# Kernel optimization log

Hardware: AMD Instinct MI355X
Metric: run time of the kernel (lower is better)

The kernel has to match this reference:

```python
import jax, jax.numpy as jnp
import numpy as np

DN = ('NHWC', 'HWIO', 'NHWC')

def _conv1x1(x, k):
    # 1x1 conv, stride 1, SAME padding (channels_last)
    return jax.lax.conv_general_dilated(x, k, window_strides=(1, 1), padding='SAME', dimension_numbers=DN)

def setup_inputs() -> dict:
    key = jax.random.key(0)
    k1, k2, k3, k4, k5 = jax.random.split(key, 5)
    B, H, W, C = 4, 64, 64, 256
    c8 = C // 8
    x = jax.random.normal(k1, (B, H, W, C), dtype=jnp.float32)
    # Glorot-like scaling for stability
    kernel_f = jax.random.normal(k2, (1, 1, C, c8), dtype=jnp.float32) * (1.0 / np.sqrt(C))
    kernel_g = jax.random.normal(k3, (1, 1, C, c8), dtype=jnp.float32) * (1.0 / np.sqrt(C))
    kernel_h = jax.random.normal(k4, (1, 1, C, C), dtype=jnp.float32) * (1.0 / np.sqrt(C))
    gamma = jax.random.normal(k5, (), dtype=jnp.float32) * 0.1
    return {'x': x, 'kernel_f': kernel_f, 'kernel_g': kernel_g, 'kernel_h': kernel_h, 'gamma': gamma}

def reference(x, kernel_f, kernel_g, kernel_h, gamma):
    B, H, W, C = x.shape
    N = H * W
    f = _conv1x1(x, kernel_f).reshape(B, N, -1)   # [B, N, C/8] queries
    g = _conv1x1(x, kernel_g).reshape(B, N, -1)   # [B, N, C/8] keys
    h = _conv1x1(x, kernel_h).reshape(B, N, -1)   # [B, N, C]   values
    e = jnp.einsum('bnc,bmc->bnm', f, g)          # [B, N, N] scores
    attn = jax.nn.softmax(e, axis=-1)
    o = jnp.einsum('bnm,bmc->bnc', attn, h).reshape(B, H, W, C)
    return x + gamma * o
```

## Files before the change

kernel.cpp:

```cpp
#include <hip/hip_runtime.h>

typedef __attribute__((ext_vector_type(8))) short bf16x8;
typedef __attribute__((ext_vector_type(4))) float f32x4;
typedef __attribute__((ext_vector_type(16))) float f32x16;

__device__ __forceinline__ unsigned short f2bf(float f) {
    union { float f; unsigned u; } v; v.f = f;
    return (unsigned short)((v.u + 0x7FFFu + ((v.u >> 16) & 1u)) >> 16);
}

__device__ __forceinline__ float fexp2(float v) {
#if __has_builtin(__builtin_amdgcn_exp2f)
    return __builtin_amdgcn_exp2f(v);
#else
    float r; asm("v_exp_f32 %0, %1" : "=v"(r) : "v"(v)); return r;
#endif
}
__device__ __forceinline__ unsigned cvt_pk_bf16(float lo, float hi) {
    unsigned r;
    asm("v_cvt_pk_bf16_f32 %0, %1, %2" : "=v"(r) : "v"(lo), "v"(hi));
    return r;
}

__device__ __forceinline__ void async16(unsigned short* lds, const unsigned short* gsrc) {
    __builtin_amdgcn_global_load_lds(
        (const __attribute__((address_space(1))) void*)gsrc,
        (__attribute__((address_space(3))) void*)lds, 16, 0, 0);
}

__global__ __launch_bounds__(256) void k_wt(const float* __restrict__ kf,
                                            const float* __restrict__ kg,
                                            const float* __restrict__ kh,
                                            unsigned short* __restrict__ wt) {
    int n = blockIdx.x, t = threadIdx.x;
    const float* src; int stride, col;
    if (n < 32)      { src = kf; stride = 32;  col = n; }
    else if (n < 64) { src = kg; stride = 32;  col = n - 32; }
    else             { src = kh; stride = 256; col = n - 64; }
    float v = src[t * stride + col];
    if (n < 32) v *= 1.44269504088896341f;
    wt[n * 256 + (((t >> 3) ^ (n & 7)) << 3) + (t & 7)] = f2bf(v);
}

__global__ __launch_bounds__(512) void k_proj(const float* __restrict__ x,
                                              const unsigned short* __restrict__ wt,
                                              unsigned short* __restrict__ f,
                                              unsigned short* __restrict__ g,
                                              unsigned short* __restrict__ hT) {
    __shared__ unsigned short xs[16384];
    __shared__ unsigned short ws[2][16384];
    int t = threadIdx.x, rb = blockIdx.x;
    int w = t >> 6, lane = t & 63, q = lane >> 4, n15 = lane & 15;
    int b = rb >> 6, nbase = (rb & 63) * 64;

#pragma unroll
    for (int i = 0; i < 8; ++i) {
        int lin = i * 512 + t, row = lin >> 6, c4 = lin & 63;
        float4 v = *(const float4*)&x[(rb * 64 + row) * 256 + c4 * 4];
        ushort4 o; o.x = f2bf(v.x); o.y = f2bf(v.y); o.z = f2bf(v.z); o.w = f2bf(v.w);
        *(ushort4*)&xs[row * 256 + (((c4 >> 1) ^ (row & 7)) << 3) + ((c4 & 1) << 2)] = o;
    }
#pragma unroll
    for (int j = 0; j < 4; ++j)
        async16(&ws[0][(j * 512 + w * 64) * 8], wt + (j * 512 + t) * 8);

    for (int ct = 0; ct < 5; ++ct) {
        int cur = ct & 1, nxt = cur ^ 1;
        __syncthreads();
        if (ct < 4) {
            const unsigned short* wsrc = wt + (ct + 1) * 16384;
#pragma unroll
            for (int j = 0; j < 4; ++j)
                async16(&ws[nxt][(j * 512 + w * 64) * 8], wsrc + (j * 512 + t) * 8);
        }
        const unsigned short* wcur = ws[cur];
        f32x4 acc[2];
        acc[0] = (f32x4){0.f, 0.f, 0.f, 0.f};
        acc[1] = (f32x4){0.f, 0.f, 0.f, 0.f};

        if (ct == 0) {
            int rg = w & 3, cg = w >> 2;
#pragma unroll
            for (int kk = 0; kk < 8; ++kk) {
                bf16x8 a = *(const bf16x8*)&xs[(rg * 16 + n15) * 256
                                + ((((kk << 2) + q) ^ (n15 & 7)) << 3)];
#pragma unroll
                for (int nt = 0; nt < 2; ++nt) {
                    bf16x8 bw = *(const bf16x8*)&wcur[(cg * 32 + nt * 16 + n15) * 256
                                    + ((((kk << 2) + q) ^ (n15 & 7)) << 3)];
                    acc[nt] = __builtin_amdgcn_mfma_f32_16x16x32_bf16(a, bw, acc[nt], 0, 0, 0);
                }
            }
#pragma unroll
            for (int nt = 0; nt < 2; ++nt)
#pragma unroll
                for (int r = 0; r < 4; ++r) {
                    int grow = rb * 64 + rg * 16 + q * 4 + r;
                    int col = cg * 32 + nt * 16 + n15;
                    unsigned short v = f2bf(acc[nt][r]);
                    if (col < 32) f[grow * 32 + col] = v;
                    else          g[grow * 32 + (col - 32)] = v;
                }
        } else {
            int cg = w & 3, rg = w >> 2;
#pragma unroll
            for (int kk = 0; kk < 8; ++kk) {
                bf16x8 a = *(const bf16x8*)&wcur[(cg * 16 + n15) * 256
                                + ((((kk << 2) + q) ^ (n15 & 7)) << 3)];
#pragma unroll
                for (int nt = 0; nt < 2; ++nt) {
                    bf16x8 bx = *(const bf16x8*)&xs[(rg * 32 + nt * 16 + n15) * 256
                                    + ((((kk << 2) + q) ^ (n15 & 7)) << 3)];
                    acc[nt] = __builtin_amdgcn_mfma_f32_16x16x32_bf16(a, bx, acc[nt], 0, 0, 0);
                }
            }
#pragma unroll
            for (int nt = 0; nt < 2; ++nt)
#pragma unroll
                for (int r = 0; r < 4; ++r) {
                    int ch = (ct - 1) * 64 + cg * 16 + q * 4 + r;
                    int nloc = nbase + rg * 32 + nt * 16 + n15;
                    hT[b * 1048576 + ch * 4096 + nloc] = f2bf(acc[nt][r]);
                }
        }
    }
}

__global__ __launch_bounds__(512, 4) void k_attn(const float* __restrict__ x,
                                                 const unsigned short* __restrict__ f,
                                                 const unsigned short* __restrict__ g,
                                                 const unsigned short* __restrict__ hT,
                                                 const float* __restrict__ gamma_p,
                                                 float* __restrict__ out) {
    __shared__ unsigned short hs[3][8192];
    __shared__ unsigned short pls[2][4096];
    __shared__ float lpart[4][64];
    __shared__ __align__(16) float lrec[64];
    int t = threadIdx.x, bx = blockIdx.x;
    int b = (bx >> 1) & 3;
    int ch2 = (bx >> 3) & 1;
    int qt = ((bx & 1) << 5) | (bx >> 4);
    int qbase = qt * 64;
    int chbase = ch2 * 128;
    int w = t >> 6, l = t & 63;
    int hi = l >> 5, l31 = l & 31;
    int q = l >> 4, n15 = l & 15;
    int cb = w & 3;
    const bool is_s = (w < 4);

    bf16x8 aFB[4];
    const unsigned short* gW = g + (b * 4096 + w * 16 + n15) * 32 + q * 8;
    if (is_s) {
#pragma unroll
        for (int nt = 0; nt < 4; ++nt)
            aFB[nt] = *(const bf16x8*)&f[(b * 4096 + qbase + nt * 16 + n15) * 32 + q * 8];
    }
    bf16x8 aG, aGn;
    f32x4 lac = (f32x4){0.f, 0.f, 0.f, 0.f};
    const f32x4 zero4 = (f32x4){0.f, 0.f, 0.f, 0.f};

    const unsigned short* hsrc = hT + b * 1048576 + (chbase + (t >> 3)) * 4096
                               + (((t & 7) ^ ((t >> 3) & 7)) << 3);

    auto s_tile = [&](int buf) {
        f32x4 sa[4];
#pragma unroll
        for (int nt = 0; nt < 4; ++nt)
            sa[nt] = __builtin_amdgcn_mfma_f32_16x16x32_bf16(aG, aFB[nt], zero4, 0, 0, 0);
        int kq = w * 4 + q;
#pragma unroll
        for (int nt = 0; nt < 4; ++nt) {
#pragma unroll
            for (int r = 0; r < 4; ++r) {
                sa[nt][r] = fexp2(sa[nt][r]);
                lac[nt] += sa[nt][r];
            }
            unsigned p0 = cvt_pk_bf16(sa[nt][0], sa[nt][1]);
            unsigned p1 = cvt_pk_bf16(sa[nt][2], sa[nt][3]);
            int row = nt * 16 + n15;
            unsigned* dst = (unsigned*)&pls[buf][row * 64]
                          + (((kq >> 1) ^ (n15 & 7)) << 2) + ((kq & 1) << 1);
            dst[0] = p0; dst[1] = p1;
        }
    };

    f32x16 o0, o1;
#pragma unroll
    for (int i = 0; i < 16; ++i) { o0[i] = 0.f; o1[i] = 0.f; }

    async16(&hs[0][w * 512], hsrc);
    async16(&hs[0][4096 + w * 512], hsrc + 64 * 4096);
    async16(&hs[1][w * 512], hsrc + 64);
    async16(&hs[1][4096 + w * 512], hsrc + 64 * 4096 + 64);
    if (is_s) {
        aG  = *(const bf16x8*)&gW[0];
        aGn = *(const bf16x8*)&gW[2048];
        s_tile(0);
        aG = aGn;
        __builtin_amdgcn_sched_barrier(0);
        asm volatile("s_waitcnt vmcnt(3) lgkmcnt(0)" ::: "memory");
    } else {
        __builtin_amdgcn_sched_barrier(0);
        asm volatile("s_waitcnt vmcnt(2)" ::: "memory");
    }
    __builtin_amdgcn_s_barrier();
    __builtin_amdgcn_sched_barrier(0);

    for (int kt = 0; kt < 64; ++kt) {
        int cur = kt & 1, nxt = cur ^ 1;
        int h_cur = kt % 3, h_nxt2 = (kt + 2) % 3;
        const bool more = (kt + 2 < 64);

        if (more) {
            const unsigned short* hp = hsrc + (kt + 2) * 64;
            async16(&hs[h_nxt2][w * 512], hp);
            async16(&hs[h_nxt2][4096 + w * 512], hp + 64 * 4096);
        }

        if (is_s) {
            if (kt + 1 < 64) {
                int ktn = (kt + 2 < 64) ? kt + 2 : 63;
                aGn = *(const bf16x8*)&gW[ktn * 2048];
                s_tile(nxt);
                aG = aGn;
            }
            __builtin_amdgcn_sched_barrier(0);
            if (more) asm volatile("s_waitcnt vmcnt(3) lgkmcnt(0)" ::: "memory");
            else      asm volatile("s_waitcnt vmcnt(1) lgkmcnt(0)" ::: "memory");
        } else {
            const unsigned short* hcur = &hs[h_cur][0];
            const unsigned short* pcur = &pls[cur][0];
            __builtin_amdgcn_s_setprio(1);
#pragma unroll
            for (int ks = 0; ks < 4; ++ks) {
                int seg = (((2 * ks + hi) ^ (l31 & 7)) << 3);
                bf16x8 bH  = *(const bf16x8*)&hcur[(cb * 32 + l31) * 64 + seg];
                bf16x8 aP0 = *(const bf16x8*)&pcur[l31 * 64 + seg];
                bf16x8 aP1 = *(const bf16x8*)&pcur[(32 + l31) * 64 + seg];
                o0 = __builtin_amdgcn_mfma_f32_32x32x16_bf16(aP0, bH, o0, 0, 0, 0);
                o1 = __builtin_amdgcn_mfma_f32_32x32x16_bf16(aP1, bH, o1, 0, 0, 0);
            }
            __builtin_amdgcn_s_setprio(0);
            __builtin_amdgcn_sched_barrier(0);
            if (more) asm volatile("s_waitcnt vmcnt(2)" ::: "memory");
            else      asm volatile("s_waitcnt vmcnt(0)" ::: "memory");
        }

        __builtin_amdgcn_s_barrier();
        __builtin_amdgcn_sched_barrier(0);
    }

    if (is_s) {
#pragma unroll
        for (int nt = 0; nt < 4; ++nt) {
            float ps = lac[nt];
            ps += __shfl_xor(ps, 16);
            ps += __shfl_xor(ps, 32);
            if (q == 0) lpart[w][nt * 16 + n15] = ps;
        }
    }
    __syncthreads();
    if (t < 64) lrec[t] = 1.0f / (lpart[0][t] + lpart[1][t] + lpart[2][t] + lpart[3][t]);
    __syncthreads();
    if (!is_s) {
        float gam = *gamma_p;
        int ch = chbase + cb * 32 + l31;
#pragma unroll
        for (int qq = 0; qq < 4; ++qq) {
            int r0 = 8 * qq + 4 * hi;
            f32x4 ri0 = *(const f32x4*)&lrec[r0];
            f32x4 ri1 = *(const f32x4*)&lrec[32 + r0];
#pragma unroll
            for (int j = 0; j < 4; ++j) {
                int idx0 = (b * 4096 + qbase + r0 + j) * 256 + ch;
                int idx1 = idx0 + 32 * 256;
                out[idx0] = x[idx0] + gam * (o0[4 * qq + j] * ri0[j]);
                out[idx1] = x[idx1] + gam * (o1[4 * qq + j] * ri1[j]);
            }
        }
    }
}

extern "C" void kernel_launch(void* const* d_in, const int* in_sizes, int n_in,
                              void* d_out, int out_size, void* d_ws, size_t ws_size,
                              hipStream_t stream) {
    const float* x  = (const float*)d_in[0];
    const float* kf = (const float*)d_in[1];
    const float* kg = (const float*)d_in[2];
    const float* kh = (const float*)d_in[3];
    const float* gm = (const float*)d_in[4];
    float* out = (float*)d_out;

    char* ws = (char*)d_ws;
    unsigned short* wt = (unsigned short*)(ws);
    unsigned short* fb = (unsigned short*)(ws + 163840);
    unsigned short* gb = (unsigned short*)(ws + 1212416);
    unsigned short* hT = (unsigned short*)(ws + 2260992);

    hipLaunchKernelGGL(k_wt,   dim3(320), dim3(256), 0, stream, kf, kg, kh, wt);
    hipLaunchKernelGGL(k_proj, dim3(256), dim3(512), 0, stream, x, wt, fb, gb, hT);
    hipLaunchKernelGGL(k_attn, dim3(512), dim3(512), 0, stream, x, fb, gb, hT, gm, out);
}
```

Baseline: 144.8 us.

## Halve projection row tile to double grid and single-buffer weight tiles

The projection kernel now processes 32 rows per block instead of 64 and launches 512 blocks instead of 256. Each wave computes one MFMA tile per stage instead of two. The weight tile buffer in shared memory is single-buffered, with the next tile loaded after the current compute and an extra barrier. This aims to fill more compute units and cut shared-memory use, at the cost of losing load/compute overlap and refetching the weights for each smaller row tile.

```diff
diff --git a/kernel.cpp b/kernel.cpp
--- a/kernel.cpp
+++ b/kernel.cpp
@@ -47,82 +47,71 @@
                                               unsigned short* __restrict__ f,
                                               unsigned short* __restrict__ g,
                                               unsigned short* __restrict__ hT) {
-    __shared__ unsigned short xs[16384];
-    __shared__ unsigned short ws[2][16384];
+    __shared__ unsigned short xs[8192];
+    __shared__ unsigned short ws[16384];
     int t = threadIdx.x, rb = blockIdx.x;
     int w = t >> 6, lane = t & 63, q = lane >> 4, n15 = lane & 15;
-    int b = rb >> 6, nbase = (rb & 63) * 64;
-
-#pragma unroll
-    for (int i = 0; i < 8; ++i) {
+    int b = rb >> 7, nbase = (rb & 127) * 32;
+    int rg0 = w & 1, cg0 = w >> 1;
+    int cgh = w & 3, rgh = w >> 2;
+
+#pragma unroll
+    for (int i = 0; i < 4; ++i) {
         int lin = i * 512 + t, row = lin >> 6, c4 = lin & 63;
-        float4 v = *(const float4*)&x[(rb * 64 + row) * 256 + c4 * 4];
+        float4 v = *(const float4*)&x[(rb * 32 + row) * 256 + c4 * 4];
         ushort4 o; o.x = f2bf(v.x); o.y = f2bf(v.y); o.z = f2bf(v.z); o.w = f2bf(v.w);
         *(ushort4*)&xs[row * 256 + (((c4 >> 1) ^ (row & 7)) << 3) + ((c4 & 1) << 2)] = o;
     }
 #pragma unroll
     for (int j = 0; j < 4; ++j)
-        async16(&ws[0][(j * 512 + w * 64) * 8], wt + (j * 512 + t) * 8);
+        async16(&ws[(j * 512 + w * 64) * 8], wt + (j * 512 + t) * 8);
+    __syncthreads();
 
     for (int ct = 0; ct < 5; ++ct) {
-        int cur = ct & 1, nxt = cur ^ 1;
+        f32x4 acc = (f32x4){0.f, 0.f, 0.f, 0.f};
+        if (ct == 0) {
+#pragma unroll
+            for (int kk = 0; kk < 8; ++kk) {
+                bf16x8 a = *(const bf16x8*)&xs[(rg0 * 16 + n15) * 256
+                                + ((((kk << 2) + q) ^ (n15 & 7)) << 3)];
+                bf16x8 bw = *(const bf16x8*)&ws[(cg0 * 16 + n15) * 256
+                                + ((((kk << 2) + q) ^ (n15 & 7)) << 3)];
+                acc = __builtin_amdgcn_mfma_f32_16x16x32_bf16(a, bw, acc, 0, 0, 0);
+            }
+        } else {
+#pragma unroll
+            for (int kk = 0; kk < 8; ++kk) {
+                bf16x8 a = *(const bf16x8*)&ws[(cgh * 16 + n15) * 256
+                                + ((((kk << 2) + q) ^ (n15 & 7)) << 3)];
+                bf16x8 bx = *(const bf16x8*)&xs[(rgh * 16 + n15) * 256
+                                + ((((kk << 2) + q) ^ (n15 & 7)) << 3)];
+                acc = __builtin_amdgcn_mfma_f32_16x16x32_bf16(a, bx, acc, 0, 0, 0);
+            }
+        }
         __syncthreads();
         if (ct < 4) {
             const unsigned short* wsrc = wt + (ct + 1) * 16384;
 #pragma unroll
             for (int j = 0; j < 4; ++j)
-                async16(&ws[nxt][(j * 512 + w * 64) * 8], wsrc + (j * 512 + t) * 8);
-        }
-        const unsigned short* wcur = ws[cur];
-        f32x4 acc[2];
-        acc[0] = (f32x4){0.f, 0.f, 0.f, 0.f};
-        acc[1] = (f32x4){0.f, 0.f, 0.f, 0.f};
-
+                async16(&ws[(j * 512 + w * 64) * 8], wsrc + (j * 512 + t) * 8);
+        }
         if (ct == 0) {
-            int rg = w & 3, cg = w >> 2;
-#pragma unroll
-            for (int kk = 0; kk < 8; ++kk) {
-                bf16x8 a = *(const bf16x8*)&xs[(rg * 16 + n15) * 256
-                                + ((((kk << 2) + q) ^ (n15 & 7)) << 3)];
-#pragma unroll
-                for (int nt = 0; nt < 2; ++nt) {
-                    bf16x8 bw = *(const bf16x8*)&wcur[(cg * 32 + nt * 16 + n15) * 256
-                                    + ((((kk << 2) + q) ^ (n15 & 7)) << 3)];
-                    acc[nt] = __builtin_amdgcn_mfma_f32_16x16x32_bf16(a, bw, acc[nt], 0, 0, 0);
-                }
-            }
-#pragma unroll
-            for (int nt = 0; nt < 2; ++nt)
-#pragma unroll
-                for (int r = 0; r < 4; ++r) {
-                    int grow = rb * 64 + rg * 16 + q * 4 + r;
-                    int col = cg * 32 + nt * 16 + n15;
-                    unsigned short v = f2bf(acc[nt][r]);
-                    if (col < 32) f[grow * 32 + col] = v;
-                    else          g[grow * 32 + (col - 32)] = v;
-                }
+#pragma unroll
+            for (int r = 0; r < 4; ++r) {
+                int grow = rb * 32 + rg0 * 16 + q * 4 + r;
+                int col = cg0 * 16 + n15;
+                unsigned short v = f2bf(acc[r]);
+                if (col < 32) f[grow * 32 + col] = v;
+                else          g[grow * 32 + (col - 32)] = v;
+            }
         } else {
-            int cg = w & 3, rg = w >> 2;
-#pragma unroll
-            for (int kk = 0; kk < 8; ++kk) {
-                bf16x8 a = *(const bf16x8*)&wcur[(cg * 16 + n15) * 256
-                                + ((((kk << 2) + q) ^ (n15 & 7)) << 3)];
-#pragma unroll
-                for (int nt = 0; nt < 2; ++nt) {
-                    bf16x8 bx = *(const bf16x8*)&xs[(rg * 32 + nt * 16 + n15) * 256
-                                    + ((((kk << 2) + q) ^ (n15 & 7)) << 3)];
-                    acc[nt] = __builtin_amdgcn_mfma_f32_16x16x32_bf16(a, bx, acc[nt], 0, 0, 0);
-                }
-            }
-#pragma unroll
-            for (int nt = 0; nt < 2; ++nt)
-#pragma unroll
-                for (int r = 0; r < 4; ++r) {
-                    int ch = (ct - 1) * 64 + cg * 16 + q * 4 + r;
-                    int nloc = nbase + rg * 32 + nt * 16 + n15;
-                    hT[b * 1048576 + ch * 4096 + nloc] = f2bf(acc[nt][r]);
-                }
-        }
+#pragma unroll
+            for (int r = 0; r < 4; ++r) {
+                int ch = (ct - 1) * 64 + cgh * 16 + q * 4 + r;
+                hT[b * 1048576 + ch * 4096 + nbase + rgh * 16 + n15] = f2bf(acc[r]);
+            }
+        }
+        __syncthreads();
     }
 }
 
@@ -298,6 +287,6 @@
     unsigned short* hT = (unsigned short*)(ws + 2260992);
 
     hipLaunchKernelGGL(k_wt,   dim3(320), dim3(256), 0, stream, kf, kg, kh, wt);
-    hipLaunchKernelGGL(k_proj, dim3(256), dim3(512), 0, stream, x, wt, fb, gb, hT);
+    hipLaunchKernelGGL(k_proj, dim3(512), dim3(512), 0, stream, x, wt, fb, gb, hT);
     hipLaunchKernelGGL(k_attn, dim3(512), dim3(512), 0, stream, x, fb, gb, hT, gm, out);
 }
```

Result: slower. 151.2 us (+4.4%).
